# Kernel optimization log

Measured on AMD Instinct MI355X. Metric: run time of the kernel, lower is better.

Reference implementation:

```python
import jax, jax.numpy as jnp
import numpy as np

B, N, D, C, H = 32, 36, 2048, 4, 512  # batch, regions, feat dim, coord dim, fusion hidden


def setup_inputs() -> dict:
    key = jax.random.key(0)
    ks = jax.random.split(key, 8)
    w = lambda k, sh: jax.random.normal(k, sh, dtype=jnp.float32) * 0.02
    return {
        "mm": jax.random.normal(ks[0], (B, N, D), dtype=jnp.float32),
        "coords": jax.random.uniform(ks[1], (B, N, C), dtype=jnp.float32),
        # MLB fusion params for coords: z = (x@W_cl * y@W_cr) @ W_cout
        "W_cl": w(ks[2], (C, H)),
        "W_cr": w(ks[3], (C, H)),
        "W_cout": w(ks[4], (H, D)),
        # MLB fusion params for features
        "W_fl": w(ks[5], (D, H)),
        "W_fr": w(ks[6], (D, H)),
        "W_fout": w(ks[7], (H, D)),
    }


def reference(mm, coords, W_cl, W_cr, W_cout, W_fl, W_fr, W_fout):
    # Project once per region (avoids projecting inside the N*N expand).
    cl = coords @ W_cl            # [B,N,H]
    cr = coords @ W_cr            # [B,N,H]
    fl = mm @ W_fl                # [B,N,H]
    fr = mm @ W_fr                # [B,N,H]
    # All-pairs bilinear fusion: Rij = f_coord(c_i, c_j) + f_feat(m_i, m_j)
    pair_c = cl[:, :, None, :] * cr[:, None, :, :]   # [B,N,N,H]
    pair_f = fl[:, :, None, :] * fr[:, None, :, :]   # [B,N,N,H]
    Rij = (jnp.einsum('bijh,hd->bijd', pair_c, W_cout)
           + jnp.einsum('bijh,hd->bijd', pair_f, W_fout))  # [B,N,N,D]
    # agg['type'] == 'max': reduce over the right (j) region axis
    mm_new = Rij.max(axis=2)      # [B,N,D]
    # residual
    return mm_new + mm
```

## Files before the change

kernel.cpp:

```cpp
#include <hip/hip_runtime.h>


typedef __attribute__((ext_vector_type(8))) short short8;
typedef __attribute__((ext_vector_type(4))) short short4v;
typedef __attribute__((ext_vector_type(4))) float f32x4;

__device__ __forceinline__ float bf2f(unsigned short h) {
  return __uint_as_float(((unsigned int)h) << 16);
}
__device__ __forceinline__ unsigned short f2bf(float f) {
  unsigned int u = __float_as_uint(f);
  u += 0x7FFFu + ((u >> 16) & 1u);
  return (unsigned short)(u >> 16);
}
__device__ __forceinline__ void gl2lds16(const void* g, void* l) {
  __builtin_amdgcn_global_load_lds(
      (const __attribute__((address_space(1))) unsigned int*)g,
      (__attribute__((address_space(3))) unsigned int*)l, 16, 0, 0);
}

__global__ __launch_bounds__(256) void k_mc(
    const float* __restrict__ Wcl, const float* __restrict__ Wcr,
    const float* __restrict__ Wcout, float* __restrict__ Mc) {
  const int d = blockIdx.x * 256 + threadIdx.x;
  float acc[16];
#pragma unroll
  for (int i = 0; i < 16; ++i) acc[i] = 0.f;
  for (int h = 0; h < 512; ++h) {
    float wo = Wcout[(size_t)h * 2048 + d];
    float cl[4], cr[4];
#pragma unroll
    for (int a = 0; a < 4; ++a) {
      cl[a] = Wcl[a * 512 + h];
      cr[a] = Wcr[a * 512 + h];
    }
#pragma unroll
    for (int a = 0; a < 4; ++a) {
      float t = cl[a] * wo;
#pragma unroll
      for (int b = 0; b < 4; ++b) acc[a * 4 + b] += t * cr[b];
    }
  }
#pragma unroll
  for (int ab = 0; ab < 16; ++ab) Mc[(size_t)ab * 2048 + d] = acc[ab];
}

__global__ __launch_bounds__(256) void k_prep(
    const float* __restrict__ mm, const float* __restrict__ Wfout,
    const float* __restrict__ Mc, const float* __restrict__ Wfl,
    const float* __restrict__ Wfr, unsigned short* __restrict__ mmb,
    unsigned short* __restrict__ WS, unsigned short* __restrict__ WS2) {
  const int bid = blockIdx.x;
  if (bid < 2304) {
    int idx = bid * 256 + threadIdx.x;
    int row = idx >> 9, h = idx & 511;
    float4 m4 = *(const float4*)(mm + (size_t)row * 2048 + h * 4);
    short4v o;
    o[0] = (short)f2bf(m4.x); o[1] = (short)f2bf(m4.y);
    o[2] = (short)f2bf(m4.z); o[3] = (short)f2bf(m4.w);
    *(short4v*)(mmb + (size_t)row * 2048 + h * 4) = o;
  } else {
    int gi = (bid - 2304) * 256 + threadIdx.x;
    if (gi < 139264) {
      int n = gi & 15, qv = (gi >> 4) & 3, rest = gi >> 6;
      int kc = rest % 17, g2 = rest / 17;
      int d = g2 * 16 + n;
      short8 o;
      if (kc < 16) {
        int kbase = kc * 32 + qv * 8;
        const float* src = Wfout + (size_t)kbase * 2048 + d;
#pragma unroll
        for (int e = 0; e < 8; ++e) o[e] = (short)f2bf(src[(size_t)e * 2048]);
      } else if (qv < 2) {
        const float* src = Mc + (size_t)(qv * 8) * 2048 + d;
#pragma unroll
        for (int e = 0; e < 8; ++e) o[e] = (short)f2bf(src[(size_t)e * 2048]);
      } else {
#pragma unroll
        for (int e = 0; e < 8; ++e) o[e] = 0;
      }
      *(short8*)(WS + (size_t)gi * 8) = o;
    } else {
      int gj = gi - 139264;
      int n = gj & 15, qv = (gj >> 4) & 3, kc = (gj >> 6) & 63, cg = gj >> 12;
      int col = cg * 16 + n;
      int dbase = kc * 32 + qv * 8;
      const float* src = (col < 512) ? (Wfl + (size_t)dbase * 512 + col)
                                     : (Wfr + (size_t)dbase * 512 + (col - 512));
      short8 o;
#pragma unroll
      for (int e = 0; e < 8; ++e) o[e] = (short)f2bf(src[(size_t)e * 512]);
      *(short8*)(WS2 + (size_t)gj * 8) = o;
    }
  }
}

__global__ __launch_bounds__(256) void k_proj_feat(
    const unsigned short* __restrict__ mmb, const unsigned short* __restrict__ WS2,
    unsigned short* __restrict__ Fl, unsigned short* __restrict__ Fr) {
  const int tid = threadIdx.x;
  const int lane = tid & 63, w = tid >> 6;
  const int n = lane & 15, q = lane >> 4;
  const int m0 = blockIdx.y * 16;
  const int cg = blockIdx.x * 4 + w;
  const int c0 = cg * 16;

  f32x4 acc = {0.f, 0.f, 0.f, 0.f};
#pragma unroll 4
  for (int kc = 0; kc < 64; ++kc) {
    short8 a = *(const short8*)(mmb + (size_t)(m0 + n) * 2048 + kc * 32 + q * 8);
    short8 b = *(const short8*)(WS2 + (size_t)(cg * 64 + kc) * 512 + lane * 8);
    acc = __builtin_amdgcn_mfma_f32_16x16x32_bf16(a, b, acc, 0, 0, 0);
  }
#pragma unroll
  for (int e = 0; e < 4; ++e) {
    int row = m0 + q * 4 + e;
    int col = c0 + n;
    unsigned short v = f2bf(acc[e]);
    if (col < 512) Fl[(size_t)row * 512 + col] = v;
    else           Fr[(size_t)row * 512 + (col - 512)] = v;
  }
}

__global__ __launch_bounds__(256) void k_prod(
    const unsigned short* __restrict__ Fl, const unsigned short* __restrict__ Fr,
    const float* __restrict__ coords, unsigned short* __restrict__ Pf) {
  int idx = blockIdx.x * 256 + threadIdx.x;
  int lane = idx & 63;
  int gran = idx >> 6;
  int qg = gran / 153;
  int rem = gran - qg * 153;
  int kc = rem / 9;
  int t = rem - kc * 9;
  int n = lane & 15, q = lane >> 4;
  int b = qg / 9;
  int g, j;
  if (t < 8) { g = qg * 4 + (t >> 1); j = (t & 1) * 16 + n; }
  else       { g = qg * 4 + (n >> 2); j = 32 + (n & 3); }
  int rowj = b * 36 + j;
  short8 p;
  if (kc < 16) {
    int k0 = kc * 32 + q * 8;
    short8 cl8 = *(const short8*)(Fl + (size_t)g * 512 + k0);
    short8 cr8 = *(const short8*)(Fr + (size_t)rowj * 512 + k0);
#pragma unroll
    for (int e = 0; e < 8; ++e)
      p[e] = (short)f2bf(bf2f((unsigned short)cl8[e]) * bf2f((unsigned short)cr8[e]));
  } else if (q < 2) {
    float4 ci = *(const float4*)(coords + (size_t)g * 4);
    float4 cj = *(const float4*)(coords + (size_t)rowj * 4);
#pragma unroll
    for (int e = 0; e < 8; ++e) {
      int a = q * 2 + (e >> 2);
      float ca = (a == 0) ? ci.x : (a == 1) ? ci.y : (a == 2) ? ci.z : ci.w;
      float cb = ((e & 3) == 0) ? cj.x : ((e & 3) == 1) ? cj.y
               : ((e & 3) == 2) ? cj.z : cj.w;
      p[e] = (short)f2bf(ca * cb);
    }
  } else {
#pragma unroll
    for (int e = 0; e < 8; ++e) p[e] = 0;
  }
  *(short8*)(Pf + (size_t)idx * 8) = p;
}

__global__ __launch_bounds__(512, 4) void k_pairwise(
    const unsigned short* __restrict__ Pf, const unsigned short* __restrict__ WS,
    const float* __restrict__ mm, float* __restrict__ out) {
  __shared__ __align__(16) unsigned short lB[2][9 * 512];

  const int tid = threadIdx.x;
  const int lane = tid & 63, w = tid >> 6;
  const int n = lane & 15, q = lane >> 4;
  const int bx = blockIdx.x;
  const int dt = bx & 7, qg = bx >> 3;
  const int g0 = qg * 4;

  f32x4 acc[9][2];
#pragma unroll
  for (int t = 0; t < 9; ++t)
#pragma unroll
    for (int r = 0; r < 2; ++r) acc[t][r] = (f32x4){0.f, 0.f, 0.f, 0.f};

  const unsigned short* Abase = WS + ((size_t)(dt * 16 + w * 2) * 17) * 512 + lane * 8;
  const unsigned short* Bbase = Pf + (size_t)qg * 17 * 9 * 512;

  short8 aR[2], aN[2];
  gl2lds16(Bbase + (size_t)w * 512 + lane * 8, &lB[0][w * 512]);
  if (w == 0) gl2lds16(Bbase + (size_t)8 * 512 + lane * 8, &lB[0][8 * 512]);
  aR[0] = *(const short8*)(Abase);
  aR[1] = *(const short8*)(Abase + 17 * 512);
  __syncthreads();

#pragma unroll 2
  for (int kc = 0; kc < 16; ++kc) {
    const int buf = kc & 1;
    const unsigned short* bn = Bbase + (size_t)((kc + 1) * 9) * 512 + lane * 8;
    gl2lds16(bn + (size_t)w * 512, &lB[buf ^ 1][w * 512]);
    if (w == 0) gl2lds16(bn + (size_t)8 * 512, &lB[buf ^ 1][8 * 512]);
    aN[0] = *(const short8*)(Abase + (size_t)(kc + 1) * 512);
    aN[1] = *(const short8*)(Abase + (size_t)(17 + kc + 1) * 512);

    short8 bb[9];
#pragma unroll
    for (int t = 0; t < 9; ++t)
      bb[t] = *(const short8*)(&lB[buf][t * 512 + lane * 8]);
#pragma unroll
    for (int t = 0; t < 9; ++t) {
      acc[t][0] = __builtin_amdgcn_mfma_f32_16x16x32_bf16(aR[0], bb[t], acc[t][0], 0, 0, 0);
      acc[t][1] = __builtin_amdgcn_mfma_f32_16x16x32_bf16(aR[1], bb[t], acc[t][1], 0, 0, 0);
    }
    __syncthreads();
    aR[0] = aN[0];
    aR[1] = aN[1];
  }

  {
    short8 bb[9];
#pragma unroll
    for (int t = 0; t < 9; ++t)
      bb[t] = *(const short8*)(&lB[0][t * 512 + lane * 8]);
#pragma unroll
    for (int t = 0; t < 9; ++t) {
      acc[t][0] = __builtin_amdgcn_mfma_f32_16x16x32_bf16(aR[0], bb[t], acc[t][0], 0, 0, 0);
      acc[t][1] = __builtin_amdgcn_mfma_f32_16x16x32_bf16(aR[1], bb[t], acc[t][1], 0, 0, 0);
    }
  }

#pragma unroll
  for (int r = 0; r < 2; ++r) {
#pragma unroll
    for (int e = 0; e < 4; ++e) {
      float vs = acc[8][r][e];
#pragma unroll
      for (int ii = 0; ii < 4; ++ii) {
        float v = fmaxf(acc[ii * 2][r][e], acc[ii * 2 + 1][r][e]);
        v = fmaxf(v, ((n >> 2) == ii) ? vs : -1e30f);
#pragma unroll
        for (int s = 1; s < 16; s <<= 1) v = fmaxf(v, __shfl_xor(v, s, 64));
        if (n == 0) {
          int d = dt * 256 + w * 32 + r * 16 + q * 4 + e;
          size_t o = (size_t)(g0 + ii) * 2048 + d;
          out[o] = v + mm[o];
        }
      }
    }
  }
}

extern "C" void kernel_launch(void* const* d_in, const int* in_sizes, int n_in,
                              void* d_out, int out_size, void* d_ws, size_t ws_size,
                              hipStream_t stream) {
  const float* mm     = (const float*)d_in[0];
  const float* coords = (const float*)d_in[1];
  const float* Wcl    = (const float*)d_in[2];
  const float* Wcr    = (const float*)d_in[3];
  const float* Wcout  = (const float*)d_in[4];
  const float* Wfl    = (const float*)d_in[5];
  const float* Wfr    = (const float*)d_in[6];
  const float* Wfout  = (const float*)d_in[7];
  float* out = (float*)d_out;

  float* Mc = (float*)d_ws;
  unsigned short* Fl  = (unsigned short*)(Mc + 16 * 2048);
  unsigned short* Fr  = Fl + (size_t)1152 * 512;
  unsigned short* WS  = Fr + (size_t)1152 * 512;
  unsigned short* WS2 = WS + (size_t)139264 * 8;
  unsigned short* mmb = WS2 + (size_t)262144 * 8;
  unsigned short* Pf  = mmb + (size_t)1152 * 2048;

  k_mc<<<8, 256, 0, stream>>>(Wcl, Wcr, Wcout, Mc);
  k_prep<<<2304 + 1568, 256, 0, stream>>>(mm, Wfout, Mc, Wfl, Wfr, mmb, WS, WS2);
  k_proj_feat<<<dim3(16, 72), 256, 0, stream>>>(mmb, WS2, Fl, Fr);
  k_prod<<<11016, 256, 0, stream>>>(Fl, Fr, coords, Pf);
  k_pairwise<<<2304, 512, 0, stream>>>(Pf, WS, mm, out);
}
```

Measured before the change: 328.5 us.

## Fuse coord-weight precompute into prep kernel and remap pairwise block indices

Removes the separate k_mc launch by computing the folded coordinate weight matrix (Wcl x Wcr x Wcout) directly inside k_prep, in the threads that pack it into bf16. This saves a launch and the serial dependency, but those threads now run a 512-iteration loop while the other prep threads do light work, which can create a tail. The pairwise kernel's block-to-(d-tile, query-group) mapping is also changed so that blocks scheduled close together share different B panels, aiming for better cache or XCD locality.

```diff
diff --git a/kernel.cpp b/kernel.cpp
--- a/kernel.cpp
+++ b/kernel.cpp
@@ -19,35 +19,10 @@
       (__attribute__((address_space(3))) unsigned int*)l, 16, 0, 0);
 }
 
-__global__ __launch_bounds__(256) void k_mc(
-    const float* __restrict__ Wcl, const float* __restrict__ Wcr,
-    const float* __restrict__ Wcout, float* __restrict__ Mc) {
-  const int d = blockIdx.x * 256 + threadIdx.x;
-  float acc[16];
-#pragma unroll
-  for (int i = 0; i < 16; ++i) acc[i] = 0.f;
-  for (int h = 0; h < 512; ++h) {
-    float wo = Wcout[(size_t)h * 2048 + d];
-    float cl[4], cr[4];
-#pragma unroll
-    for (int a = 0; a < 4; ++a) {
-      cl[a] = Wcl[a * 512 + h];
-      cr[a] = Wcr[a * 512 + h];
-    }
-#pragma unroll
-    for (int a = 0; a < 4; ++a) {
-      float t = cl[a] * wo;
-#pragma unroll
-      for (int b = 0; b < 4; ++b) acc[a * 4 + b] += t * cr[b];
-    }
-  }
-#pragma unroll
-  for (int ab = 0; ab < 16; ++ab) Mc[(size_t)ab * 2048 + d] = acc[ab];
-}
-
 __global__ __launch_bounds__(256) void k_prep(
     const float* __restrict__ mm, const float* __restrict__ Wfout,
-    const float* __restrict__ Mc, const float* __restrict__ Wfl,
+    const float* __restrict__ Wcl, const float* __restrict__ Wcr,
+    const float* __restrict__ Wcout, const float* __restrict__ Wfl,
     const float* __restrict__ Wfr, unsigned short* __restrict__ mmb,
     unsigned short* __restrict__ WS, unsigned short* __restrict__ WS2) {
   const int bid = blockIdx.x;
@@ -72,9 +47,22 @@
 #pragma unroll
         for (int e = 0; e < 8; ++e) o[e] = (short)f2bf(src[(size_t)e * 2048]);
       } else if (qv < 2) {
-        const float* src = Mc + (size_t)(qv * 8) * 2048 + d;
-#pragma unroll
-        for (int e = 0; e < 8; ++e) o[e] = (short)f2bf(src[(size_t)e * 2048]);
+        float acc[8];
+#pragma unroll
+        for (int e = 0; e < 8; ++e) acc[e] = 0.f;
+        for (int h = 0; h < 512; ++h) {
+          float wo = Wcout[(size_t)h * 2048 + d];
+          float c0 = Wcl[(qv * 2 + 0) * 512 + h] * wo;
+          float c1 = Wcl[(qv * 2 + 1) * 512 + h] * wo;
+          float r0 = Wcr[h], r1 = Wcr[512 + h];
+          float r2 = Wcr[1024 + h], r3 = Wcr[1536 + h];
+          acc[0] += c0 * r0; acc[1] += c0 * r1;
+          acc[2] += c0 * r2; acc[3] += c0 * r3;
+          acc[4] += c1 * r0; acc[5] += c1 * r1;
+          acc[6] += c1 * r2; acc[7] += c1 * r3;
+        }
+#pragma unroll
+        for (int e = 0; e < 8; ++e) o[e] = (short)f2bf(acc[e]);
       } else {
 #pragma unroll
         for (int e = 0; e < 8; ++e) o[e] = 0;
@@ -173,7 +161,10 @@
   const int lane = tid & 63, w = tid >> 6;
   const int n = lane & 15, q = lane >> 4;
   const int bx = blockIdx.x;
-  const int dt = bx & 7, qg = bx >> 3;
+  const int x = bx & 7;
+  const int m = bx >> 3;
+  const int dt = m & 7;
+  const int qg = x * 36 + (m >> 3);
   const int g0 = qg * 4;
 
   f32x4 acc[9][2];
@@ -261,16 +252,15 @@
   const float* Wfout  = (const float*)d_in[7];
   float* out = (float*)d_out;
 
-  float* Mc = (float*)d_ws;
-  unsigned short* Fl  = (unsigned short*)(Mc + 16 * 2048);
+  unsigned short* Fl  = (unsigned short*)d_ws;
   unsigned short* Fr  = Fl + (size_t)1152 * 512;
   unsigned short* WS  = Fr + (size_t)1152 * 512;
   unsigned short* WS2 = WS + (size_t)139264 * 8;
   unsigned short* mmb = WS2 + (size_t)262144 * 8;
   unsigned short* Pf  = mmb + (size_t)1152 * 2048;
 
-  k_mc<<<8, 256, 0, stream>>>(Wcl, Wcr, Wcout, Mc);
-  k_prep<<<2304 + 1568, 256, 0, stream>>>(mm, Wfout, Mc, Wfl, Wfr, mmb, WS, WS2);
+  k_prep<<<2304 + 1568, 256, 0, stream>>>(mm, Wfout, Wcl, Wcr, Wcout,
+                                          Wfl, Wfr, mmb, WS, WS2);
   k_proj_feat<<<dim3(16, 72), 256, 0, stream>>>(mmb, WS2, Fl, Fr);
   k_prod<<<11016, 256, 0, stream>>>(Fl, Fr, coords, Pf);
   k_pairwise<<<2304, 512, 0, stream>>>(Pf, WS, mm, out);
```

New measurement: 293.4 us. -10.7%, faster.
